# Optimization experiments

Hardware: AMD Instinct MI355X
Metric: run time of the kernel (lower is better)

## Reference

```python
import jax, jax.numpy as jnp
import numpy as np

KS = 9          # ms_ks in the original module
PAD = KS // 2   # conv padding along H
B, C, H, W = 32, 1, 384, 1280


def _corr_h(col, w):
    """9-tap cross-correlation along H with zero padding.
    col: [B, H], w: [KS] -> [B, H]. Matches torch Conv2d(1,1,(9,1),padding=(4,0))
    applied to a [B,1,H,1] column."""
    p = jnp.pad(col, ((0, 0), (PAD, PAD)))
    acc = w[0] * p[:, 0:H]
    for k in range(1, KS):  # static unroll over the 9 taps
        acc = acc + w[k] * p[:, k:k + H]
    return acc


def _scan_pass(xs, w, reverse):
    """Sequential message passing over columns.
    xs: [W, B, H]; out[i] = xs[i] + relu(corr(out[i-1], w)), out[0] = xs[0]."""
    if reverse:
        xs = xs[::-1]

    def step(carry, xcol):
        new = xcol + jax.nn.relu(_corr_h(carry, w))
        return new, new

    _, outs = jax.lax.scan(step, xs[0], xs[1:])
    out = jnp.concatenate([xs[:1], outs], axis=0)
    if reverse:
        out = out[::-1]
    return out


def setup_inputs() -> dict:
    key = jax.random.key(0)
    k1, k2, k3 = jax.random.split(key, 3)
    x = jax.random.uniform(k1, (B, C, H, W), dtype=jnp.float32)  # sigmoid disparity in [0,1]
    bound = 1.0 / np.sqrt(KS)  # torch Conv2d default init bound (fan_in = 1*9*1)
    w_lr = jax.random.uniform(k2, (KS,), dtype=jnp.float32, minval=-bound, maxval=bound)
    w_rl = jax.random.uniform(k3, (KS,), dtype=jnp.float32, minval=-bound, maxval=bound)
    return {"x": x, "w_lr": w_lr, "w_rl": w_rl}


def reference(x, w_lr, w_rl):
    # x: [B, 1, H, W] -> columns-first [W, B, H]
    xs = jnp.transpose(x[:, 0], (2, 0, 1))
    xs = _scan_pass(xs, w_lr, reverse=False)  # left -> right
    xs = _scan_pass(xs, w_rl, reverse=True)   # right -> left
    return jnp.transpose(xs, (1, 2, 0))[:, None, :, :]  # [B, 1, H, W]
```

## Files before the change

kernel.cpp:

```cpp
#include <hip/hip_runtime.h>

#define BB 32
#define HH 384
#define WW 1280
#define KS 9
#define NT 256
#define NPAIR 192
#define BSTR ((size_t)WW * NPAIR)

typedef float f2v __attribute__((ext_vector_type(2)));
typedef float4 f4;

static __device__ __forceinline__ f2v pk_mul(f2v a, f2v b) {
    f2v d; asm("v_pk_mul_f32 %0, %1, %2" : "=v"(d) : "v"(a), "v"(b)); return d;
}
static __device__ __forceinline__ f2v pk_fma(f2v a, f2v b, f2v c) {
    f2v d; asm("v_pk_fma_f32 %0, %1, %2, %3" : "=v"(d) : "v"(a), "v"(b), "v"(c)); return d;
}
static __device__ __forceinline__ float du(float v) {
    return __int_as_float(__builtin_amdgcn_mov_dpp(__float_as_int(v), 0x138, 0xf, 0xf, true));
}
static __device__ __forceinline__ float dd(float v) {
    return __int_as_float(__builtin_amdgcn_mov_dpp(__float_as_int(v), 0x130, 0xf, 0xf, true));
}
template<int U> __device__ __forceinline__ void setc(f4& q, float v) {
    if constexpr (U == 0) q.x = v;
    else if constexpr (U == 1) q.y = v;
    else if constexpr (U == 2) q.z = v;
    else q.w = v;
}

__global__ __launch_bounds__(512) void scnn_tr(const float* __restrict__ x,
                                               f2v* __restrict__ xq) {
    __shared__ float tile[HH][33];
    const int b = blockIdx.y;
    const int c0 = blockIdx.x * 32;
    const int t = threadIdx.x;
    const int col = t & 31;
    const int r0 = t >> 5;
    const float* xb = x + (size_t)b * HH * WW + c0;
#pragma unroll
    for (int k = 0; k < 24; ++k) {
        const int r = r0 + 16 * k;
        tile[r][col] = xb[(size_t)r * WW + col];
    }
    __syncthreads();
    f2v* xqb = xq + (size_t)b * BSTR + (size_t)c0 * NPAIR;
#pragma unroll
    for (int i = 0; i < 12; ++i) {
        const int idx = i * 512 + t;
        const int cl = idx / NPAIR;
        const int pp = idx - cl * NPAIR;
        f2v v;
        v.x = tile[2 * pp][cl];
        v.y = tile[2 * pp + 1][cl];
        xqb[(size_t)cl * NPAIR + pp] = v;
    }
}

static __device__ __forceinline__ f2v conv9(const f2v V, const f2v (&W)[KS]) {
    f2v A1, A0, A3, A4;
    A1.x = du(V.x);  A1.y = du(V.y);
    A0.x = du(A1.x); A0.y = du(A1.y);
    A3.x = dd(V.x);  A3.y = dd(V.y);
    A4.x = dd(A3.x); A4.y = dd(A3.y);
    f2v a = pk_mul(W[0], A0);
    a = pk_fma(W[2], A1, a);
    a = pk_fma(W[4], V,  a);
    a = pk_fma(W[6], A3, a);
    a = pk_fma(W[8], A4, a);
    float ax = a.x, ay = a.y;
    ax = fmaf(W[1].x, A0.y, ax);
    ax = fmaf(W[3].x, A1.y, ax);
    ax = fmaf(W[5].x, V.y,  ax);
    ax = fmaf(W[7].x, A3.y, ax);
    ay = fmaf(W[1].x, A1.x, ay);
    ay = fmaf(W[3].x, V.x,  ay);
    ay = fmaf(W[5].x, A3.x, ay);
    ay = fmaf(W[7].x, A4.x, ay);
    f2v r; r.x = fmaxf(ax, 0.f); r.y = fmaxf(ay, 0.f);
    return r;
}

__global__ __launch_bounds__(NT, 1) void scnn_scan(f2v* __restrict__ xq,
                                                   float* __restrict__ out,
                                                   const float* __restrict__ w_lr,
                                                   const float* __restrict__ w_rl) {
    __shared__ f2v lb[2][NPAIR];
    __shared__ f2v lx[2][NPAIR][4];

    const int b   = blockIdx.x;
    const int tid = threadIdx.x;
    const int wid = tid >> 6;
    const int l   = tid & 63;
    const int p   = 48 * wid - 8 + l;
    const bool inb   = (p >= 0) && (p < NPAIR);
    const bool owned = (l >= 8) && (l < 56);
    const int pc = p < 0 ? 0 : (p > NPAIR - 1 ? NPAIR - 1 : p);
    const int plo = 48 * wid, phi = 48 * wid + 47;
    const int po = p < plo ? plo : (p > phi ? phi : p);

    f2v* xb = xq + (size_t)b * BSTR;
    float* outb = out + (size_t)b * HH * WW;

    f2v Wl[KS], Wr[KS];
#pragma unroll
    for (int k = 0; k < KS; ++k) {
        const float a = w_lr[k], c = w_rl[k];
        Wl[k].x = a; Wl[k].y = a;
        Wr[k].x = c; Wr[k].y = c;
    }

    int par = 0;
    f2v V;

#define MASKV(v) do { (v).x = inb ? (v).x : 0.f; (v).y = inb ? (v).y : 0.f; } while (0)

#define STEP1(XV, COL) do { \
    f2v _a = conv9(V, Wl); \
    V.x = (XV).x + _a.x; V.y = (XV).y + _a.y; \
    MASKV(V); \
    if (owned) xb[(size_t)(COL) * NPAIR + p] = V; \
} while (0)

#define REFRESH1(S) do { \
    if (owned) { \
        lb[par][p] = V; \
        lx[par][p][0] = Xr[(S) + 0]; lx[par][p][1] = Xr[(S) + 1]; \
        lx[par][p][2] = Xr[(S) + 2]; lx[par][p][3] = Xr[(S) + 3]; \
    } \
    asm volatile("s_waitcnt lgkmcnt(0)\n\ts_barrier" ::: "memory"); \
    { f2v _t = lb[par][pc]; \
      f2v _x0 = lx[par][pc][0], _x1 = lx[par][pc][1]; \
      f2v _x2 = lx[par][pc][2], _x3 = lx[par][pc][3]; \
      V.x = inb ? _t.x : 0.f; V.y = inb ? _t.y : 0.f; \
      if (!owned) { Xr[(S)+0] = _x0; Xr[(S)+1] = _x1; Xr[(S)+2] = _x2; Xr[(S)+3] = _x3; } \
    } \
    par ^= 1; \
} while (0)

#define REFRESH2() do { \
    if (owned) lb[par][p] = V; \
    asm volatile("s_waitcnt lgkmcnt(0)\n\ts_barrier" ::: "memory"); \
    { f2v _t = lb[par][pc]; V.x = inb ? _t.x : 0.f; V.y = inb ? _t.y : 0.f; } \
    par ^= 1; \
} while (0)

    {
        f2v Xr[8];
#pragma unroll
        for (int u = 0; u < 8; ++u) Xr[u] = xb[(size_t)(1 + u) * NPAIR + po];
        V = xb[po];
        MASKV(V);
        REFRESH1(0);
#pragma unroll 1
        for (int m = 0; m < 159; ++m) {
            const int q = 8 * m + 1;
            STEP1(Xr[0], q + 0); STEP1(Xr[1], q + 1);
            STEP1(Xr[2], q + 2); STEP1(Xr[3], q + 3);
            Xr[0] = xb[(size_t)(q + 8  > WW-1 ? WW-1 : q + 8 ) * NPAIR + po];
            Xr[1] = xb[(size_t)(q + 9  > WW-1 ? WW-1 : q + 9 ) * NPAIR + po];
            Xr[2] = xb[(size_t)(q + 10 > WW-1 ? WW-1 : q + 10) * NPAIR + po];
            Xr[3] = xb[(size_t)(q + 11 > WW-1 ? WW-1 : q + 11) * NPAIR + po];
            REFRESH1(4);
            STEP1(Xr[4], q + 4); STEP1(Xr[5], q + 5);
            STEP1(Xr[6], q + 6); STEP1(Xr[7], q + 7);
            Xr[4] = xb[(size_t)(q + 12 > WW-1 ? WW-1 : q + 12) * NPAIR + po];
            Xr[5] = xb[(size_t)(q + 13 > WW-1 ? WW-1 : q + 13) * NPAIR + po];
            Xr[6] = xb[(size_t)(q + 14 > WW-1 ? WW-1 : q + 14) * NPAIR + po];
            Xr[7] = xb[(size_t)(q + 15 > WW-1 ? WW-1 : q + 15) * NPAIR + po];
            REFRESH1(0);
        }
        STEP1(Xr[0], 1273); STEP1(Xr[1], 1274);
        STEP1(Xr[2], 1275); STEP1(Xr[3], 1276);
        REFRESH1(4);
        STEP1(Xr[4], 1277); STEP1(Xr[5], 1278); STEP1(Xr[6], 1279);
    }

    __syncthreads();

    {
        f2v Or[8];
#pragma unroll
        for (int u = 0; u < 8; ++u) Or[u] = xb[(size_t)(1278 - u) * NPAIR + pc];
        REFRESH2();

        f4 obE[2], obO[2];

#define STEP2(C8, OV) do { \
    f2v _a = conv9(V, Wr); \
    V.x = (OV).x + _a.x; V.y = (OV).y + _a.y; \
    MASKV(V); \
    setc<(C8) & 3>(obE[(C8) >> 2], V.x); \
    setc<(C8) & 3>(obO[(C8) >> 2], V.y); \
} while (0)

#define FLUSH(W8) do { \
    if (owned) { \
        float* _r0 = outb + (size_t)(2 * p) * WW + (W8); \
        *(f4*)_r0 = obE[0]; *(f4*)(_r0 + 4) = obE[1]; \
        float* _r1 = _r0 + WW; \
        *(f4*)_r1 = obO[0]; *(f4*)(_r1 + 4) = obO[1]; \
    } \
} while (0)

        setc<3>(obE[1], V.x); setc<3>(obO[1], V.y);
#pragma unroll 1
        for (int m = 0; m < 159; ++m) {
            const int cA = 1278 - 8 * m;
            STEP2(6, Or[0]); STEP2(5, Or[1]);
            STEP2(4, Or[2]); STEP2(3, Or[3]);
            Or[0] = xb[(size_t)(cA - 8  < 0 ? 0 : cA - 8 ) * NPAIR + pc];
            Or[1] = xb[(size_t)(cA - 9  < 0 ? 0 : cA - 9 ) * NPAIR + pc];
            Or[2] = xb[(size_t)(cA - 10 < 0 ? 0 : cA - 10) * NPAIR + pc];
            Or[3] = xb[(size_t)(cA - 11 < 0 ? 0 : cA - 11) * NPAIR + pc];
            REFRESH2();
            STEP2(2, Or[4]); STEP2(1, Or[5]); STEP2(0, Or[6]);
            FLUSH(cA - 6);
            STEP2(7, Or[7]);
            Or[4] = xb[(size_t)(cA - 12 < 0 ? 0 : cA - 12) * NPAIR + pc];
            Or[5] = xb[(size_t)(cA - 13 < 0 ? 0 : cA - 13) * NPAIR + pc];
            Or[6] = xb[(size_t)(cA - 14 < 0 ? 0 : cA - 14) * NPAIR + pc];
            Or[7] = xb[(size_t)(cA - 15 < 0 ? 0 : cA - 15) * NPAIR + pc];
            REFRESH2();
        }
        STEP2(6, Or[0]); STEP2(5, Or[1]);
        STEP2(4, Or[2]); STEP2(3, Or[3]);
        REFRESH2();
        STEP2(2, Or[4]); STEP2(1, Or[5]); STEP2(0, Or[6]);
        FLUSH(0);
    }
}

extern "C" void kernel_launch(void* const* d_in, const int* in_sizes, int n_in,
                              void* d_out, int out_size, void* d_ws, size_t ws_size,
                              hipStream_t stream) {
    const float* x    = (const float*)d_in[0];
    const float* w_lr = (const float*)d_in[1];
    const float* w_rl = (const float*)d_in[2];
    float* out = (float*)d_out;
    f2v*   xq  = (f2v*)d_ws;

    scnn_tr<<<dim3(WW / 32, BB), 512, 0, stream>>>(x, xq);
    scnn_scan<<<BB, NT, 0, stream>>>(xq, out, w_lr, w_rl);
}
```

Baseline: 426.9 us.

## Give each lane two row-pairs and widen halo to cut barrier frequency

Each lane now holds two adjacent row pairs (four rows) instead of one, and the per-wave halo grows to 20 lanes. That lets each wave run 20 column steps between LDS exchange barriers instead of 4, and global loads and stores become float4. The forward pass now writes to a separate buffer instead of overwriting the transposed input in place, with a fallback that writes through the workspace and adds a copy kernel when the workspace is too small. The cost is more redundant halo computation per wave, more register pressure, and possibly an extra full-size copy kernel.

Result: faster. 398.9 us (-6.5%).

```diff
diff --git a/kernel.cpp b/kernel.cpp
--- a/kernel.cpp
+++ b/kernel.cpp
@@ -23,6 +23,8 @@
 static __device__ __forceinline__ float dd(float v) {
     return __int_as_float(__builtin_amdgcn_mov_dpp(__float_as_int(v), 0x130, 0xf, 0xf, true));
 }
+static __device__ __forceinline__ f2v du2(f2v v) { f2v r; r.x = du(v.x); r.y = du(v.y); return r; }
+static __device__ __forceinline__ f2v dd2(f2v v) { f2v r; r.x = dd(v.x); r.y = dd(v.y); return r; }
 template<int U> __device__ __forceinline__ void setc(f4& q, float v) {
     if constexpr (U == 0) q.x = v;
     else if constexpr (U == 1) q.y = v;
@@ -58,50 +60,56 @@
     }
 }
 
-static __device__ __forceinline__ f2v conv9(const f2v V, const f2v (&W)[KS]) {
-    f2v A1, A0, A3, A4;
-    A1.x = du(V.x);  A1.y = du(V.y);
-    A0.x = du(A1.x); A0.y = du(A1.y);
-    A3.x = dd(V.x);  A3.y = dd(V.y);
-    A4.x = dd(A3.x); A4.y = dd(A3.y);
-    f2v a = pk_mul(W[0], A0);
-    a = pk_fma(W[2], A1, a);
-    a = pk_fma(W[4], V,  a);
-    a = pk_fma(W[6], A3, a);
-    a = pk_fma(W[8], A4, a);
+__global__ __launch_bounds__(256) void scnn_cp(const f4* __restrict__ s,
+                                               f4* __restrict__ d, int n) {
+    int i = blockIdx.x * 256 + threadIdx.x;
+    const int stride = gridDim.x * 256;
+    for (; i < n; i += stride) d[i] = s[i];
+}
+
+static __device__ __forceinline__ f2v conv5(f2v C0, f2v C1, f2v C2, f2v C3, f2v C4,
+                                            const f2v (&W)[KS]) {
+    f2v a = pk_mul(W[0], C0);
+    a = pk_fma(W[2], C1, a);
+    a = pk_fma(W[4], C2, a);
+    a = pk_fma(W[6], C3, a);
+    a = pk_fma(W[8], C4, a);
     float ax = a.x, ay = a.y;
-    ax = fmaf(W[1].x, A0.y, ax);
-    ax = fmaf(W[3].x, A1.y, ax);
-    ax = fmaf(W[5].x, V.y,  ax);
-    ax = fmaf(W[7].x, A3.y, ax);
-    ay = fmaf(W[1].x, A1.x, ay);
-    ay = fmaf(W[3].x, V.x,  ay);
-    ay = fmaf(W[5].x, A3.x, ay);
-    ay = fmaf(W[7].x, A4.x, ay);
+    ax = fmaf(W[1].x, C0.y, ax);
+    ax = fmaf(W[3].x, C1.y, ax);
+    ax = fmaf(W[5].x, C2.y, ax);
+    ax = fmaf(W[7].x, C3.y, ax);
+    ay = fmaf(W[1].x, C1.x, ay);
+    ay = fmaf(W[3].x, C2.x, ay);
+    ay = fmaf(W[5].x, C3.x, ay);
+    ay = fmaf(W[7].x, C4.x, ay);
     f2v r; r.x = fmaxf(ax, 0.f); r.y = fmaxf(ay, 0.f);
     return r;
 }
 
-__global__ __launch_bounds__(NT, 1) void scnn_scan(f2v* __restrict__ xq,
-                                                   float* __restrict__ out,
+__global__ __launch_bounds__(NT, 1) void scnn_scan(const f2v* __restrict__ xq,
+                                                   f2v* __restrict__ o1,
+                                                   float* __restrict__ fin,
                                                    const float* __restrict__ w_lr,
                                                    const float* __restrict__ w_rl) {
-    __shared__ f2v lb[2][NPAIR];
-    __shared__ f2v lx[2][NPAIR][4];
+    __shared__ float lbx[2][NPAIR], lby[2][NPAIR];
 
     const int b   = blockIdx.x;
     const int tid = threadIdx.x;
     const int wid = tid >> 6;
     const int l   = tid & 63;
-    const int p   = 48 * wid - 8 + l;
-    const bool inb   = (p >= 0) && (p < NPAIR);
-    const bool owned = (l >= 8) && (l < 56);
-    const int pc = p < 0 ? 0 : (p > NPAIR - 1 ? NPAIR - 1 : p);
-    const int plo = 48 * wid, phi = 48 * wid + 47;
-    const int po = p < plo ? plo : (p > phi ? phi : p);
-
-    f2v* xb = xq + (size_t)b * BSTR;
-    float* outb = out + (size_t)b * HH * WW;
+    const int p0  = 48 * wid - 40 + 2 * l;
+    const int p1  = p0 + 1;
+    const bool inb0 = (p0 >= 0) && (p0 < NPAIR);
+    const bool inb1 = (p1 >= 0) && (p1 < NPAIR);
+    const bool owned = (l >= 20) && (l < 44);
+    const int p0x = p0 < 0 ? 0 : (p0 > NPAIR - 2 ? NPAIR - 2 : p0);
+    const int p1x = p0x + 1;
+    const int R0 = 2 * p0;
+
+    const f2v* xqb = xq + (size_t)b * BSTR;
+    f2v*       o1b = o1 + (size_t)b * BSTR;
+    float*     finb = fin + (size_t)b * HH * WW;
 
     f2v Wl[KS], Wr[KS];
 #pragma unroll
@@ -112,123 +120,123 @@
     }
 
     int par = 0;
-    f2v V;
-
-#define MASKV(v) do { (v).x = inb ? (v).x : 0.f; (v).y = inb ? (v).y : 0.f; } while (0)
-
-#define STEP1(XV, COL) do { \
-    f2v _a = conv9(V, Wl); \
-    V.x = (XV).x + _a.x; V.y = (XV).y + _a.y; \
-    MASKV(V); \
-    if (owned) xb[(size_t)(COL) * NPAIR + p] = V; \
-} while (0)
-
-#define REFRESH1(S) do { \
+    f2v S0, S1;
+    f4 XR[10];
+
+#define REFRESH() do { \
+    if (owned) { lbx[par][p0] = S0.x; lby[par][p0] = S0.y; \
+                 lbx[par][p1] = S1.x; lby[par][p1] = S1.y; } \
+    asm volatile("s_waitcnt lgkmcnt(0)\n\ts_barrier" ::: "memory"); \
+    { float a0 = lbx[par][p0x], b0 = lby[par][p0x]; \
+      float a1 = lbx[par][p1x], b1 = lby[par][p1x]; \
+      S0.x = inb0 ? a0 : 0.f; S0.y = inb0 ? b0 : 0.f; \
+      S1.x = inb1 ? a1 : 0.f; S1.y = inb1 ? b1 : 0.f; } \
+    par ^= 1; \
+} while (0)
+
+#define STEP1(COL, XI) do { \
+    f2v U0 = du2(S0), U1 = du2(S1), D0 = dd2(S0), D1 = dd2(S1); \
+    f2v A0 = conv5(U0, U1, S0, S1, D0, Wl); \
+    f2v A1 = conv5(U1, S0, S1, D0, D1, Wl); \
+    f4 xv = XR[XI]; \
+    S0.x = inb0 ? (xv.x + A0.x) : 0.f;  S0.y = inb0 ? (xv.y + A0.y) : 0.f; \
+    S1.x = inb1 ? (xv.z + A1.x) : 0.f;  S1.y = inb1 ? (xv.w + A1.y) : 0.f; \
+    if (owned) { f4 sv; sv.x = S0.x; sv.y = S0.y; sv.z = S1.x; sv.w = S1.y; \
+        *(f4*)(o1b + (size_t)(COL) * NPAIR + p0) = sv; } \
+    { const int _pc = (COL) + 10 > WW - 1 ? WW - 1 : (COL) + 10; \
+      XR[XI] = *(const f4*)(xqb + (size_t)_pc * NPAIR + p0x); } \
+} while (0)
+
+    {
+        f4 v = *(const f4*)(xqb + p0x);
+        S0.x = inb0 ? v.x : 0.f; S0.y = inb0 ? v.y : 0.f;
+        S1.x = inb1 ? v.z : 0.f; S1.y = inb1 ? v.w : 0.f;
+        if (owned) { f4 sv; sv.x = S0.x; sv.y = S0.y; sv.z = S1.x; sv.w = S1.y;
+            *(f4*)(o1b + p0) = sv; }
+#pragma unroll
+        for (int i = 0; i < 10; ++i)
+            XR[i] = *(const f4*)(xqb + (size_t)(1 + i) * NPAIR + p0x);
+#pragma unroll 1
+        for (int g = 0; g < 127; ++g) {
+            if ((g & 1) == 0) REFRESH();
+            const int c0 = 1 + 10 * g;
+            STEP1(c0 + 0, 0); STEP1(c0 + 1, 1); STEP1(c0 + 2, 2); STEP1(c0 + 3, 3);
+            STEP1(c0 + 4, 4); STEP1(c0 + 5, 5); STEP1(c0 + 6, 6); STEP1(c0 + 7, 7);
+            STEP1(c0 + 8, 8); STEP1(c0 + 9, 9);
+        }
+        STEP1(1271, 0); STEP1(1272, 1); STEP1(1273, 2); STEP1(1274, 3);
+        STEP1(1275, 4); STEP1(1276, 5); STEP1(1277, 6); STEP1(1278, 7);
+        STEP1(1279, 8);
+    }
+
+    __syncthreads();
+
+    {
+        f4 ob[4];
+
+#define STEP2(COL, XI, WPOS) do { \
+    f2v U0 = du2(S0), U1 = du2(S1), D0 = dd2(S0), D1 = dd2(S1); \
+    f2v A0 = conv5(U0, U1, S0, S1, D0, Wr); \
+    f2v A1 = conv5(U1, S0, S1, D0, D1, Wr); \
+    f4 ov = XR[XI]; \
+    S0.x = inb0 ? (ov.x + A0.x) : 0.f;  S0.y = inb0 ? (ov.y + A0.y) : 0.f; \
+    S1.x = inb1 ? (ov.z + A1.x) : 0.f;  S1.y = inb1 ? (ov.w + A1.y) : 0.f; \
+    setc<WPOS>(ob[0], S0.x); setc<WPOS>(ob[1], S0.y); \
+    setc<WPOS>(ob[2], S1.x); setc<WPOS>(ob[3], S1.y); \
+    { const int _pc = (COL) - 10 < 0 ? 0 : (COL) - 10; \
+      XR[XI] = *(const f4*)(o1b + (size_t)_pc * NPAIR + p0x); } \
+} while (0)
+
+#define FLUSH(W4) do { \
     if (owned) { \
-        lb[par][p] = V; \
-        lx[par][p][0] = Xr[(S) + 0]; lx[par][p][1] = Xr[(S) + 1]; \
-        lx[par][p][2] = Xr[(S) + 2]; lx[par][p][3] = Xr[(S) + 3]; \
+        *(f4*)(finb + (size_t)(R0 + 0) * WW + (W4)) = ob[0]; \
+        *(f4*)(finb + (size_t)(R0 + 1) * WW + (W4)) = ob[1]; \
+        *(f4*)(finb + (size_t)(R0 + 2) * WW + (W4)) = ob[2]; \
+        *(f4*)(finb + (size_t)(R0 + 3) * WW + (W4)) = ob[3]; \
     } \
-    asm volatile("s_waitcnt lgkmcnt(0)\n\ts_barrier" ::: "memory"); \
-    { f2v _t = lb[par][pc]; \
-      f2v _x0 = lx[par][pc][0], _x1 = lx[par][pc][1]; \
-      f2v _x2 = lx[par][pc][2], _x3 = lx[par][pc][3]; \
-      V.x = inb ? _t.x : 0.f; V.y = inb ? _t.y : 0.f; \
-      if (!owned) { Xr[(S)+0] = _x0; Xr[(S)+1] = _x1; Xr[(S)+2] = _x2; Xr[(S)+3] = _x3; } \
-    } \
-    par ^= 1; \
-} while (0)
-
-#define REFRESH2() do { \
-    if (owned) lb[par][p] = V; \
-    asm volatile("s_waitcnt lgkmcnt(0)\n\ts_barrier" ::: "memory"); \
-    { f2v _t = lb[par][pc]; V.x = inb ? _t.x : 0.f; V.y = inb ? _t.y : 0.f; } \
-    par ^= 1; \
-} while (0)
-
-    {
-        f2v Xr[8];
-#pragma unroll
-        for (int u = 0; u < 8; ++u) Xr[u] = xb[(size_t)(1 + u) * NPAIR + po];
-        V = xb[po];
-        MASKV(V);
-        REFRESH1(0);
+} while (0)
+
+        {
+            f4 v = *(const f4*)(o1b + (size_t)(WW - 1) * NPAIR + p0x);
+            S0.x = inb0 ? v.x : 0.f; S0.y = inb0 ? v.y : 0.f;
+            S1.x = inb1 ? v.z : 0.f; S1.y = inb1 ? v.w : 0.f;
+            setc<3>(ob[0], S0.x); setc<3>(ob[1], S0.y);
+            setc<3>(ob[2], S1.x); setc<3>(ob[3], S1.y);
+#pragma unroll
+            for (int i = 0; i < 10; ++i)
+                XR[i] = *(const f4*)(o1b + (size_t)(1278 - i) * NPAIR + p0x);
+        }
 #pragma unroll 1
-        for (int m = 0; m < 159; ++m) {
-            const int q = 8 * m + 1;
-            STEP1(Xr[0], q + 0); STEP1(Xr[1], q + 1);
-            STEP1(Xr[2], q + 2); STEP1(Xr[3], q + 3);
-            Xr[0] = xb[(size_t)(q + 8  > WW-1 ? WW-1 : q + 8 ) * NPAIR + po];
-            Xr[1] = xb[(size_t)(q + 9  > WW-1 ? WW-1 : q + 9 ) * NPAIR + po];
-            Xr[2] = xb[(size_t)(q + 10 > WW-1 ? WW-1 : q + 10) * NPAIR + po];
-            Xr[3] = xb[(size_t)(q + 11 > WW-1 ? WW-1 : q + 11) * NPAIR + po];
-            REFRESH1(4);
-            STEP1(Xr[4], q + 4); STEP1(Xr[5], q + 5);
-            STEP1(Xr[6], q + 6); STEP1(Xr[7], q + 7);
-            Xr[4] = xb[(size_t)(q + 12 > WW-1 ? WW-1 : q + 12) * NPAIR + po];
-            Xr[5] = xb[(size_t)(q + 13 > WW-1 ? WW-1 : q + 13) * NPAIR + po];
-            Xr[6] = xb[(size_t)(q + 14 > WW-1 ? WW-1 : q + 14) * NPAIR + po];
-            Xr[7] = xb[(size_t)(q + 15 > WW-1 ? WW-1 : q + 15) * NPAIR + po];
-            REFRESH1(0);
+        for (int m = 0; m < 63; ++m) {
+            REFRESH();
+            const int c0 = 1278 - 20 * m;
+            STEP2(c0 - 0, 0, 2);
+            STEP2(c0 - 1, 1, 1);
+            STEP2(c0 - 2, 2, 0);  FLUSH(c0 - 2);
+            STEP2(c0 - 3, 3, 3);
+            STEP2(c0 - 4, 4, 2);
+            STEP2(c0 - 5, 5, 1);
+            STEP2(c0 - 6, 6, 0);  FLUSH(c0 - 6);
+            STEP2(c0 - 7, 7, 3);
+            STEP2(c0 - 8, 8, 2);
+            STEP2(c0 - 9, 9, 1);
+            STEP2(c0 - 10, 0, 0); FLUSH(c0 - 10);
+            STEP2(c0 - 11, 1, 3);
+            STEP2(c0 - 12, 2, 2);
+            STEP2(c0 - 13, 3, 1);
+            STEP2(c0 - 14, 4, 0); FLUSH(c0 - 14);
+            STEP2(c0 - 15, 5, 3);
+            STEP2(c0 - 16, 6, 2);
+            STEP2(c0 - 17, 7, 1);
+            STEP2(c0 - 18, 8, 0); FLUSH(c0 - 18);
+            STEP2(c0 - 19, 9, 3);
         }
-        STEP1(Xr[0], 1273); STEP1(Xr[1], 1274);
-        STEP1(Xr[2], 1275); STEP1(Xr[3], 1276);
-        REFRESH1(4);
-        STEP1(Xr[4], 1277); STEP1(Xr[5], 1278); STEP1(Xr[6], 1279);
-    }
-
-    __syncthreads();
-
-    {
-        f2v Or[8];
-#pragma unroll
-        for (int u = 0; u < 8; ++u) Or[u] = xb[(size_t)(1278 - u) * NPAIR + pc];
-        REFRESH2();
-
-        f4 obE[2], obO[2];
-
-#define STEP2(C8, OV) do { \
-    f2v _a = conv9(V, Wr); \
-    V.x = (OV).x + _a.x; V.y = (OV).y + _a.y; \
-    MASKV(V); \
-    setc<(C8) & 3>(obE[(C8) >> 2], V.x); \
-    setc<(C8) & 3>(obO[(C8) >> 2], V.y); \
-} while (0)
-
-#define FLUSH(W8) do { \
-    if (owned) { \
-        float* _r0 = outb + (size_t)(2 * p) * WW + (W8); \
-        *(f4*)_r0 = obE[0]; *(f4*)(_r0 + 4) = obE[1]; \
-        float* _r1 = _r0 + WW; \
-        *(f4*)_r1 = obO[0]; *(f4*)(_r1 + 4) = obO[1]; \
-    } \
-} while (0)
-
-        setc<3>(obE[1], V.x); setc<3>(obO[1], V.y);
-#pragma unroll 1
-        for (int m = 0; m < 159; ++m) {
-            const int cA = 1278 - 8 * m;
-            STEP2(6, Or[0]); STEP2(5, Or[1]);
-            STEP2(4, Or[2]); STEP2(3, Or[3]);
-            Or[0] = xb[(size_t)(cA - 8  < 0 ? 0 : cA - 8 ) * NPAIR + pc];
-            Or[1] = xb[(size_t)(cA - 9  < 0 ? 0 : cA - 9 ) * NPAIR + pc];
-            Or[2] = xb[(size_t)(cA - 10 < 0 ? 0 : cA - 10) * NPAIR + pc];
-            Or[3] = xb[(size_t)(cA - 11 < 0 ? 0 : cA - 11) * NPAIR + pc];
-            REFRESH2();
-            STEP2(2, Or[4]); STEP2(1, Or[5]); STEP2(0, Or[6]);
-            FLUSH(cA - 6);
-            STEP2(7, Or[7]);
-            Or[4] = xb[(size_t)(cA - 12 < 0 ? 0 : cA - 12) * NPAIR + pc];
-            Or[5] = xb[(size_t)(cA - 13 < 0 ? 0 : cA - 13) * NPAIR + pc];
-            Or[6] = xb[(size_t)(cA - 14 < 0 ? 0 : cA - 14) * NPAIR + pc];
-            Or[7] = xb[(size_t)(cA - 15 < 0 ? 0 : cA - 15) * NPAIR + pc];
-            REFRESH2();
-        }
-        STEP2(6, Or[0]); STEP2(5, Or[1]);
-        STEP2(4, Or[2]); STEP2(3, Or[3]);
-        REFRESH2();
-        STEP2(2, Or[4]); STEP2(1, Or[5]); STEP2(0, Or[6]);
-        FLUSH(0);
+        REFRESH();
+        STEP2(18, 0, 2); STEP2(17, 1, 1); STEP2(16, 2, 0); FLUSH(16);
+        STEP2(15, 3, 3); STEP2(14, 4, 2); STEP2(13, 5, 1); STEP2(12, 6, 0); FLUSH(12);
+        STEP2(11, 7, 3); STEP2(10, 8, 2); STEP2(9, 9, 1);  STEP2(8, 0, 0);  FLUSH(8);
+        STEP2(7, 1, 3);  STEP2(6, 2, 2);  STEP2(5, 3, 1);  STEP2(4, 4, 0);  FLUSH(4);
+        STEP2(3, 5, 3);  STEP2(2, 6, 2);  STEP2(1, 7, 1);  STEP2(0, 8, 0);  FLUSH(0);
     }
 }
 
@@ -238,9 +246,18 @@
     const float* x    = (const float*)d_in[0];
     const float* w_lr = (const float*)d_in[1];
     const float* w_rl = (const float*)d_in[2];
-    float* out = (float*)d_out;
+
+    const size_t half = (size_t)BB * BSTR * sizeof(f2v);
+    const bool big = ws_size >= 2 * half;
+
     f2v*   xq  = (f2v*)d_ws;
+    f2v*   o1  = big ? (f2v*)((char*)d_ws + half) : (f2v*)d_out;
+    float* fin = big ? (float*)d_out : (float*)d_ws;
 
     scnn_tr<<<dim3(WW / 32, BB), 512, 0, stream>>>(x, xq);
-    scnn_scan<<<BB, NT, 0, stream>>>(xq, out, w_lr, w_rl);
-}
+    scnn_scan<<<BB, NT, 0, stream>>>(xq, o1, fin, w_lr, w_rl);
+    if (!big) {
+        const int n4 = BB * HH * WW / 4;
+        scnn_cp<<<2048, 256, 0, stream>>>((const f4*)d_ws, (f4*)d_out, n4);
+    }
+}
```
